# Kernel optimization log

Hardware: AMD Instinct MI355X
Metric: run time of the kernel (lower is better)

## Reference

```python
import jax, jax.numpy as jnp
import numpy as np

WEIGHT_GROUP = 128  # in-channel group size for scales (module default)


def setup_inputs() -> dict:
    key = jax.random.key(0)
    k1, k2, k3, k4, k5 = jax.random.split(key, 5)
    B, IN, OUT = 16, 8192, 8192
    nG = IN // WEIGHT_GROUP  # 64 scale groups along in_features
    x = jax.random.normal(k1, (B, IN), dtype=jnp.float32)
    # 'weight' stores the already-quantized low-bit float values (small magnitudes)
    weight = jax.random.normal(k2, (OUT, IN), dtype=jnp.float32)
    # per-(row, group) positive scales
    scale_buf = jax.random.uniform(k3, (OUT, nG), dtype=jnp.float32, minval=0.01, maxval=1.0)
    bias = jax.random.normal(k4, (1, OUT), dtype=jnp.float32)
    # per-[64, group]-block mantissa-format ids in {0,1,2}; selects the dequant
    # format on hardware but is a constant lookup (no float math) in the reference
    types = jax.random.randint(k5, (OUT // 64, nG), 0, 3, dtype=jnp.int32)
    return {"x": x, "weight": weight, "scale_buf": scale_buf, "bias": bias, "types": types}


def reference(x, weight, scale_buf, bias, types):
    O, I = weight.shape
    nG = scale_buf.shape[1]
    G = I // nG
    # group-wise dequant: w_deq[o, g*G + j] = weight[o, g*G + j] * scale_buf[o, g]
    w_deq = (weight.reshape(O, nG, G) * scale_buf[:, :, None]).reshape(O, I)
    # y = x @ W_deq^T + bias   [B, O]
    return jnp.einsum("bi,oi->bo", x, w_deq) + bias
```

## Files before the change

### kernel.cpp

```cpp
#include <hip/hip_runtime.h>
#include <hip/hip_bf16.h>

#define IN_F 8192
#define OUT_F 8192
#define NB 16
#define NG 64
#define KSPLIT 8
#define KRANGE (IN_F / KSPLIT)
#define NSTEP (KRANGE / 32)

typedef __attribute__((ext_vector_type(8))) short bf16x8;
typedef __attribute__((ext_vector_type(4))) float f32x4;

static __device__ __forceinline__ short f2bf(float f) {
    __hip_bfloat16 h = __float2bfloat16(f);
    return *reinterpret_cast<short*>(&h);
}

__global__ __launch_bounds__(256)
void init_out_kernel(const float* __restrict__ bias, float* __restrict__ out) {
    const int i = blockIdx.x * 256 + threadIdx.x;
    out[i] = bias[i & (OUT_F - 1)];
}

__global__ __launch_bounds__(256, 4)
void axcore_mfma_kernel(const float* __restrict__ x,
                        const float* __restrict__ w,
                        const float* __restrict__ scale,
                        float* __restrict__ out) {
    __shared__ __align__(16) unsigned short xswz[NSTEP * 64 * 8];

    const int t    = threadIdx.x;
    const int wv   = t >> 6;
    const int lane = t & 63;
    const int k0   = blockIdx.y * KRANGE;
    const int o0   = blockIdx.x * 64 + wv * 16;

#pragma unroll
    for (int p = 0; p < 16; ++p) {
        const int idx = p * 256 + t;
        const int m   = idx >> 8;
        const int k4  = (idx & 255) * 4;
        const float4 v = *(const float4*)&x[m * IN_F + k0 + k4];
        const int tt = k4 >> 5;
        const int ln = m + 16 * ((k4 & 31) >> 3);
        const int jj = k4 & 7;
        ushort4 sv;
        sv.x = (unsigned short)f2bf(v.x);
        sv.y = (unsigned short)f2bf(v.y);
        sv.z = (unsigned short)f2bf(v.z);
        sv.w = (unsigned short)f2bf(v.w);
        *(ushort4*)&xswz[(tt * 64 + ln) * 8 + jj] = sv;
    }
    __syncthreads();

    const int nrow = o0 + (lane & 15);
    const int koct = (lane >> 4) * 8;
    const float* wrow = &w[(size_t)nrow * IN_F];

    const float4 sA = *(const float4*)&scale[nrow * NG + (k0 >> 7)];
    const float4 sB = *(const float4*)&scale[nrow * NG + (k0 >> 7) + 4];
    float sg[8] = {sA.x, sA.y, sA.z, sA.w, sB.x, sB.y, sB.z, sB.w};

    f32x4 acc = {0.f, 0.f, 0.f, 0.f};

#pragma unroll 2
    for (int gi = 0; gi < KRANGE / 128; ++gi) {
        const float s = sg[gi];
#pragma unroll
        for (int ts = 0; ts < 4; ++ts) {
            const int tt = gi * 4 + ts;
            const int kg = k0 + tt * 32 + koct;
            const float4 w0 = *(const float4*)&wrow[kg];
            const float4 w1 = *(const float4*)&wrow[kg + 4];

            bf16x8 bfrag;
            bfrag[0] = f2bf(w0.x * s);
            bfrag[1] = f2bf(w0.y * s);
            bfrag[2] = f2bf(w0.z * s);
            bfrag[3] = f2bf(w0.w * s);
            bfrag[4] = f2bf(w1.x * s);
            bfrag[5] = f2bf(w1.y * s);
            bfrag[6] = f2bf(w1.z * s);
            bfrag[7] = f2bf(w1.w * s);

            const bf16x8 afrag = *(const bf16x8*)&xswz[(tt * 64 + lane) * 8];

            acc = __builtin_amdgcn_mfma_f32_16x16x32_bf16(afrag, bfrag, acc,
                                                          0, 0, 0);
        }
    }

#pragma unroll
    for (int r = 0; r < 4; ++r) {
        const int b = (lane >> 4) * 4 + r;
        atomicAdd(&out[b * OUT_F + nrow], acc[r]);
    }
}

extern "C" void kernel_launch(void* const* d_in, const int* in_sizes, int n_in,
                              void* d_out, int out_size, void* d_ws, size_t ws_size,
                              hipStream_t stream) {
    const float* x    = (const float*)d_in[0];
    const float* w    = (const float*)d_in[1];
    const float* sc   = (const float*)d_in[2];
    const float* bias = (const float*)d_in[3];
    float* out = (float*)d_out;

    hipLaunchKernelGGL(init_out_kernel, dim3(NB * OUT_F / 256), dim3(256),
                       0, stream, bias, out);
    hipLaunchKernelGGL(axcore_mfma_kernel, dim3(OUT_F / 64, KSPLIT), dim3(256),
                       0, stream, x, w, sc, out);
}
```

Baseline: 403.0 us.

## Software-prefetch weight rows in registers and use cheaper bf16 packing

The K loop is fully unrolled and the fp32 weight loads move into an 8-deep register ring buffer, so global loads are issued well ahead of their MFMA use and memory latency is hidden in this bandwidth-bound GEMV. The library fp32-to-bf16 conversion is replaced with an add-0x8000 plus byte-permute pack of two values. That pack rounds half-up instead of round-to-nearest-even and does not handle NaN. The deeper prefetch also raises register pressure under launch_bounds(256,4).

```diff
diff --git a/kernel.cpp b/kernel.cpp
--- a/kernel.cpp
+++ b/kernel.cpp
@@ -8,13 +8,15 @@
 #define KSPLIT 8
 #define KRANGE (IN_F / KSPLIT)
 #define NSTEP (KRANGE / 32)
+#define PF 8
 
 typedef __attribute__((ext_vector_type(8))) short bf16x8;
 typedef __attribute__((ext_vector_type(4))) float f32x4;
 
-static __device__ __forceinline__ short f2bf(float f) {
-    __hip_bfloat16 h = __float2bfloat16(f);
-    return *reinterpret_cast<short*>(&h);
+static __device__ __forceinline__ unsigned bfpack2(float a, float b) {
+    unsigned ua = __float_as_uint(a) + 0x8000u;
+    unsigned ub = __float_as_uint(b) + 0x8000u;
+    return __builtin_amdgcn_perm(ub, ua, 0x07060302u);
 }
 
 __global__ __launch_bounds__(256)
@@ -31,10 +33,9 @@
     __shared__ __align__(16) unsigned short xswz[NSTEP * 64 * 8];
 
     const int t    = threadIdx.x;
-    const int wv   = t >> 6;
     const int lane = t & 63;
     const int k0   = blockIdx.y * KRANGE;
-    const int o0   = blockIdx.x * 64 + wv * 16;
+    const int o0   = blockIdx.x * 64 + (t >> 6) * 16;
 
 #pragma unroll
     for (int p = 0; p < 16; ++p) {
@@ -45,50 +46,50 @@
         const int tt = k4 >> 5;
         const int ln = m + 16 * ((k4 & 31) >> 3);
         const int jj = k4 & 7;
-        ushort4 sv;
-        sv.x = (unsigned short)f2bf(v.x);
-        sv.y = (unsigned short)f2bf(v.y);
-        sv.z = (unsigned short)f2bf(v.z);
-        sv.w = (unsigned short)f2bf(v.w);
-        *(ushort4*)&xswz[(tt * 64 + ln) * 8 + jj] = sv;
+        uint2 sv;
+        sv.x = bfpack2(v.x, v.y);
+        sv.y = bfpack2(v.z, v.w);
+        *(uint2*)&xswz[(tt * 64 + ln) * 8 + jj] = sv;
     }
     __syncthreads();
 
     const int nrow = o0 + (lane & 15);
     const int koct = (lane >> 4) * 8;
-    const float* wrow = &w[(size_t)nrow * IN_F];
+    const float* wrow = &w[(size_t)nrow * IN_F + k0 + koct];
 
     const float4 sA = *(const float4*)&scale[nrow * NG + (k0 >> 7)];
     const float4 sB = *(const float4*)&scale[nrow * NG + (k0 >> 7) + 4];
-    float sg[8] = {sA.x, sA.y, sA.z, sA.w, sB.x, sB.y, sB.z, sB.w};
+    const float sg[8] = {sA.x, sA.y, sA.z, sA.w, sB.x, sB.y, sB.z, sB.w};
+
+    float4 wbuf0[PF], wbuf1[PF];
+#pragma unroll
+    for (int i = 0; i < PF; ++i) {
+        wbuf0[i] = *(const float4*)&wrow[i * 32];
+        wbuf1[i] = *(const float4*)&wrow[i * 32 + 4];
+    }
 
     f32x4 acc = {0.f, 0.f, 0.f, 0.f};
 
-#pragma unroll 2
-    for (int gi = 0; gi < KRANGE / 128; ++gi) {
-        const float s = sg[gi];
 #pragma unroll
-        for (int ts = 0; ts < 4; ++ts) {
-            const int tt = gi * 4 + ts;
-            const int kg = k0 + tt * 32 + koct;
-            const float4 w0 = *(const float4*)&wrow[kg];
-            const float4 w1 = *(const float4*)&wrow[kg + 4];
+    for (int ts = 0; ts < NSTEP; ++ts) {
+        const float4 w0 = wbuf0[ts % PF];
+        const float4 w1 = wbuf1[ts % PF];
+        if (ts + PF < NSTEP) {
+            wbuf0[ts % PF] = *(const float4*)&wrow[(ts + PF) * 32];
+            wbuf1[ts % PF] = *(const float4*)&wrow[(ts + PF) * 32 + 4];
+        }
+        const float s = sg[ts / 4];
 
-            bf16x8 bfrag;
-            bfrag[0] = f2bf(w0.x * s);
-            bfrag[1] = f2bf(w0.y * s);
-            bfrag[2] = f2bf(w0.z * s);
-            bfrag[3] = f2bf(w0.w * s);
-            bfrag[4] = f2bf(w1.x * s);
-            bfrag[5] = f2bf(w1.y * s);
-            bfrag[6] = f2bf(w1.z * s);
-            bfrag[7] = f2bf(w1.w * s);
+        bf16x8 bfrag;
+        unsigned* bu = (unsigned*)&bfrag;
+        bu[0] = bfpack2(w0.x * s, w0.y * s);
+        bu[1] = bfpack2(w0.z * s, w0.w * s);
+        bu[2] = bfpack2(w1.x * s, w1.y * s);
+        bu[3] = bfpack2(w1.z * s, w1.w * s);
 
-            const bf16x8 afrag = *(const bf16x8*)&xswz[(tt * 64 + lane) * 8];
+        const bf16x8 afrag = *(const bf16x8*)&xswz[(ts * 64 + lane) * 8];
 
-            acc = __builtin_amdgcn_mfma_f32_16x16x32_bf16(afrag, bfrag, acc,
-                                                          0, 0, 0);
-        }
+        acc = __builtin_amdgcn_mfma_f32_16x16x32_bf16(afrag, bfrag, acc, 0, 0, 0);
     }
 
 #pragma unroll
```

Result: no change. 395.8 us (-1.8%).
